# Optimization experiments

Measured on AMD Instinct MI355X. Metric: run time of the kernel, lower is better.

Reference implementation:

```python
import jax, jax.numpy as jnp
import numpy as np

# ---- config (matches init_kwargs) ----
B, L = 2, 4096
HID = 2048            # hidden_size
N_HEADS = 16          # (max_ngram_size-1) * n_head_per_ngram = 2*8
D_HEAD = 64           # n_embed_per_ngram // n_head_per_ngram
ENG = 1024            # (max_ngram_size-1) * n_embed_per_ngram
VOCAB = 129280        # per-head hash vocab
HC = 4                # hc_mult
K = 4                 # kernel_size
DIL = 3               # dilation = max_ngram_size
EPS_RMS = 1.1920929e-07   # torch RMSNorm default eps (fp32 finfo eps)
EPS_SC = 1e-05            # ShortConv RMSNorm eps


def setup_inputs() -> dict:
    key = jax.random.key(0)
    ks = jax.random.split(key, 10)
    hidden_states = jax.random.normal(ks[0], (B, L, HID), dtype=jnp.float32)
    hash_ids = jax.random.randint(ks[1], (B, L, N_HEADS), 0, VOCAB, dtype=jnp.int64)
    emb_tables = jax.random.normal(ks[2], (N_HEADS, VOCAB, D_HEAD), dtype=jnp.float32) * 0.02
    value_w = jax.random.normal(ks[3], (ENG, HID), dtype=jnp.float32) * (1.0 / np.sqrt(ENG))
    value_b = jnp.zeros((HID,), dtype=jnp.float32)
    key_w = jax.random.normal(ks[4], (HC, ENG, HID), dtype=jnp.float32) * (1.0 / np.sqrt(ENG))
    key_b = jnp.zeros((HC, HID), dtype=jnp.float32)
    norm1_w = jnp.ones((HC, HID), dtype=jnp.float32)
    norm2_w = jnp.ones((HC, HID), dtype=jnp.float32)
    sc_norm_w = jnp.ones((HC, HID), dtype=jnp.float32)
    conv_w = jax.random.normal(ks[5], (HC * HID, 1, K), dtype=jnp.float32) * (1.0 / np.sqrt(K))
    return {
        'hidden_states': hidden_states, 'hash_ids': hash_ids,
        'emb_tables': emb_tables, 'value_w': value_w, 'value_b': value_b,
        'key_w': key_w, 'key_b': key_b, 'norm1_w': norm1_w, 'norm2_w': norm2_w,
        'sc_norm_w': sc_norm_w, 'conv_w': conv_w,
    }


def _rms(x, w, eps):
    # x: [..., D], w broadcastable to x
    var = jnp.mean(x * x, axis=-1, keepdims=True)
    return x * jax.lax.rsqrt(var + eps) * w


def _short_conv(val, sc_norm_w, conv_w):
    # val: [B, L, HC, HID]
    xn = _rms(val, sc_norm_w[None, None, :, :], EPS_SC)          # per-channel RMSNorm
    x_bct = xn.reshape(B, L, HC * HID).transpose(0, 2, 1)        # [B, C, T]
    pad = (K - 1) * DIL                                          # causal left pad
    y = jax.lax.conv_general_dilated(
        x_bct, conv_w, window_strides=(1,), padding=[(pad, 0)],
        rhs_dilation=(DIL,), dimension_numbers=('NCH', 'OIH', 'NCH'),
        feature_group_count=HC * HID)                            # depthwise
    y = jax.nn.silu(y)
    return y.transpose(0, 2, 1).reshape(B, L, HC, HID)


def reference(hidden_states, hash_ids, emb_tables, value_w, value_b,
              key_w, key_b, norm1_w, norm2_w, sc_norm_w, conv_w):
    # multi-head embedding gather: per head its own table -> [B, L, H, Dh]
    emb = jax.vmap(lambda tab, ids: tab[ids], in_axes=(0, 2), out_axes=2)(emb_tables, hash_ids)
    emb = emb.reshape(B, L, ENG)                                 # flatten heads

    # per-channel key projections and gate computation
    keys = jnp.einsum('ble,geh->blgh', emb, key_w) + key_b[None, None]   # [B,L,HC,HID]
    nk = _rms(keys, norm1_w[None, None], EPS_RMS)
    nq = _rms(hidden_states[:, :, None, :], norm2_w[None, None], EPS_RMS)
    gate = jnp.sum(nk * nq, axis=-1) / np.sqrt(HID)              # [B,L,HC]
    gate = jnp.sign(gate) * jnp.sqrt(jnp.maximum(jnp.abs(gate), 1e-06))
    gate = jax.nn.sigmoid(gate)[..., None]                       # [B,L,HC,1]

    value = gate * (emb @ value_w + value_b)[:, :, None, :]      # [B,L,HC,HID]
    out = value + _short_conv(value, sc_norm_w, conv_w)
    return out.sum(axis=2)                                       # [B,L,HID]
```

## Files before the change

kernel.cpp:

```cpp
#include <hip/hip_runtime.h>
#include <math.h>

#define LQ 4096
#define MTOK 8192
#define HID 2048
#define NHEADS 16
#define DHEAD 64
#define ENG 1024
#define VOCAB 129280
#define HC 4
#define EPS_RMS 1.1920929e-07f
#define EPS_SC  1e-05f
#define INV_SQRT_HID 0.022097086912079608f

typedef __bf16 bf16;
typedef __attribute__((ext_vector_type(8))) __bf16 bf16x8;
typedef __attribute__((ext_vector_type(4))) __bf16 bf16x4;
typedef __attribute__((ext_vector_type(4))) float f32x4;

#define AS1 __attribute__((address_space(1)))
#define AS3 __attribute__((address_space(3)))

__device__ __forceinline__ void gl_lds16(const void* g, void* l) {
    __builtin_amdgcn_global_load_lds((const AS1 unsigned int*)g,
                                     (AS3 unsigned int*)l, 16, 0, 0);
}

__global__ __launch_bounds__(256) void gather_kernel(
        const int* __restrict__ hash_ids,
        const float* __restrict__ emb_tables,
        bf16* __restrict__ emb)
{
    int t = blockIdx.x;
    int tid = threadIdx.x;
    const int* ids = hash_ids + (size_t)t * NHEADS;
    int k = tid * 4;
    int h = k >> 6, d = k & 63;
    int id = ids[h];
    float4 v = *(const float4*)(emb_tables + ((size_t)h * VOCAB + (size_t)id) * DHEAD + d);
    bf16x4 o = {(bf16)v.x, (bf16)v.y, (bf16)v.z, (bf16)v.w};
    *(bf16x4*)(emb + (size_t)t * ENG + k) = o;
}

__global__ __launch_bounds__(256) void transpose_kernel(
        const float* __restrict__ value_w,
        const float* __restrict__ key_w,
        bf16* __restrict__ vwT,
        bf16* __restrict__ kwT)
{
    __shared__ float tile[32][33];
    int z = blockIdx.z;
    const float* src = (z == 0) ? value_w : key_w + (size_t)(z - 1) * ENG * HID;
    bf16* dst = (z == 0) ? vwT : kwT + (size_t)(z - 1) * HID * ENG;
    int c0 = blockIdx.x * 32, r0 = blockIdx.y * 32;
    int tx = threadIdx.x & 31, ty = threadIdx.x >> 5;
    #pragma unroll
    for (int i = 0; i < 4; ++i)
        tile[ty + i * 8][tx] = src[(size_t)(r0 + ty + i * 8) * HID + c0 + tx];
    __syncthreads();
    #pragma unroll
    for (int i = 0; i < 4; ++i)
        dst[(size_t)(c0 + ty + i * 8) * ENG + r0 + tx] = (bf16)tile[tx][ty + i * 8];
}

__global__ __launch_bounds__(256, 1) void gemm_value_mfma(
        const bf16* __restrict__ A,
        const bf16* __restrict__ Bt,
        const float* __restrict__ bias,
        float* __restrict__ C,
        float* __restrict__ pv2)
{
    __shared__ __align__(16) bf16 sA[128 * 64];
    __shared__ __align__(16) bf16 sB[128 * 64];
    int tid = threadIdx.x;
    int L = tid & 63, w = tid >> 6;
    int m0 = blockIdx.y * 128, n0 = blockIdx.x * 128;
    int mw = (w & 1) * 64, nw = (w >> 1) * 64;
    int lrow = L >> 3;
    int kcS = ((L & 7) ^ lrow) * 8;
    int lane15 = L & 15, quad = L >> 4;

    f32x4 acc[4][4];
    #pragma unroll
    for (int fm = 0; fm < 4; ++fm)
        #pragma unroll
        for (int fn = 0; fn < 4; ++fn)
            acc[fm][fn] = (f32x4){0.f, 0.f, 0.f, 0.f};

    for (int k0 = 0; k0 < ENG; k0 += 64) {
        #pragma unroll
        for (int i = 0; i < 4; ++i) {
            int seg = w * 4 + i;
            gl_lds16(A + (size_t)(m0 + seg * 8 + lrow) * ENG + k0 + kcS, sA + seg * 512);
            gl_lds16(Bt + (size_t)(n0 + seg * 8 + lrow) * ENG + k0 + kcS, sB + seg * 512);
        }
        __syncthreads();
        #pragma unroll
        for (int ks = 0; ks < 2; ++ks) {
            bf16x8 af[4], bfr[4];
            int kc = ks * 4 + quad;
            #pragma unroll
            for (int f = 0; f < 4; ++f) {
                int ra = mw + f * 16 + lane15;
                int rb = nw + f * 16 + lane15;
                af[f]  = *(const bf16x8*)(sA + ra * 64 + ((kc ^ (ra & 7)) * 8));
                bfr[f] = *(const bf16x8*)(sB + rb * 64 + ((kc ^ (rb & 7)) * 8));
            }
            #pragma unroll
            for (int fm = 0; fm < 4; ++fm)
                #pragma unroll
                for (int fn = 0; fn < 4; ++fn)
                    acc[fm][fn] = __builtin_amdgcn_mfma_f32_16x16x32_bf16(
                        af[fm], bfr[fn], acc[fm][fn], 0, 0, 0);
        }
        __syncthreads();
    }
    #pragma unroll
    for (int fm = 0; fm < 4; ++fm) {
        #pragma unroll
        for (int r = 0; r < 4; ++r) {
            int m = m0 + mw + fm * 16 + quad * 4 + r;
            float sv = 0.f;
            #pragma unroll
            for (int fn = 0; fn < 4; ++fn) {
                int n = n0 + nw + fn * 16 + lane15;
                float v = acc[fm][fn][r] + bias[n];
                C[(size_t)m * HID + n] = v;
                sv += v * v;
            }
            sv += __shfl_xor(sv, 1); sv += __shfl_xor(sv, 2);
            sv += __shfl_xor(sv, 4); sv += __shfl_xor(sv, 8);
            if (lane15 == 0) atomicAdd(&pv2[m], sv);
        }
    }
}

__global__ __launch_bounds__(256, 1) void gemm_keys_mfma(
        const bf16* __restrict__ A,
        const bf16* __restrict__ kwT,
        const float* __restrict__ key_b,
        const float* __restrict__ hidden,
        const float* __restrict__ w1,
        const float* __restrict__ w2,
        float* __restrict__ p_sq,
        float* __restrict__ p_dot)
{
    __shared__ __align__(16) bf16 sA[128 * 64];
    __shared__ __align__(16) bf16 sB[128 * 64];
    int tid = threadIdx.x;
    int L = tid & 63, w = tid >> 6;
    int m0 = blockIdx.y * 128;
    int c0 = blockIdx.x * 128;
    int g = c0 >> 11;
    int nc0 = c0 & (HID - 1);
    const bf16* Bt = kwT + (size_t)g * HID * ENG;
    int mw = (w & 1) * 64, nw = (w >> 1) * 64;
    int lrow = L >> 3;
    int kcS = ((L & 7) ^ lrow) * 8;
    int lane15 = L & 15, quad = L >> 4;

    f32x4 acc[4][4];
    #pragma unroll
    for (int fm = 0; fm < 4; ++fm)
        #pragma unroll
        for (int fn = 0; fn < 4; ++fn)
            acc[fm][fn] = (f32x4){0.f, 0.f, 0.f, 0.f};

    for (int k0 = 0; k0 < ENG; k0 += 64) {
        #pragma unroll
        for (int i = 0; i < 4; ++i) {
            int seg = w * 4 + i;
            gl_lds16(A  + (size_t)(m0  + seg * 8 + lrow) * ENG + k0 + kcS, sA + seg * 512);
            gl_lds16(Bt + (size_t)(nc0 + seg * 8 + lrow) * ENG + k0 + kcS, sB + seg * 512);
        }
        __syncthreads();
        #pragma unroll
        for (int ks = 0; ks < 2; ++ks) {
            bf16x8 af[4], bfr[4];
            int kc = ks * 4 + quad;
            #pragma unroll
            for (int f = 0; f < 4; ++f) {
                int ra = mw + f * 16 + lane15;
                int rb = nw + f * 16 + lane15;
                af[f]  = *(const bf16x8*)(sA + ra * 64 + ((kc ^ (ra & 7)) * 8));
                bfr[f] = *(const bf16x8*)(sB + rb * 64 + ((kc ^ (rb & 7)) * 8));
            }
            #pragma unroll
            for (int fm = 0; fm < 4; ++fm)
                #pragma unroll
                for (int fn = 0; fn < 4; ++fn)
                    acc[fm][fn] = __builtin_amdgcn_mfma_f32_16x16x32_bf16(
                        af[fm], bfr[fn], acc[fm][fn], 0, 0, 0);
        }
        __syncthreads();
    }
    const float* kb = key_b + (size_t)g * HID;
    const float* w1g = w1 + (size_t)g * HID;
    const float* w2g = w2 + (size_t)g * HID;
    #pragma unroll
    for (int fm = 0; fm < 4; ++fm) {
        #pragma unroll
        for (int r = 0; r < 4; ++r) {
            int m = m0 + mw + fm * 16 + quad * 4 + r;
            float psq = 0.f, pdt = 0.f;
            #pragma unroll
            for (int fn = 0; fn < 4; ++fn) {
                int nc = nc0 + nw + fn * 16 + lane15;
                float v = acc[fm][fn][r] + kb[nc];
                float hv = hidden[(size_t)m * HID + nc];
                float ww = w1g[nc] * w2g[nc];
                psq += v * v;
                pdt += v * hv * ww;
            }
            psq += __shfl_xor(psq, 1); psq += __shfl_xor(psq, 2);
            psq += __shfl_xor(psq, 4); psq += __shfl_xor(psq, 8);
            pdt += __shfl_xor(pdt, 1); pdt += __shfl_xor(pdt, 2);
            pdt += __shfl_xor(pdt, 4); pdt += __shfl_xor(pdt, 8);
            if (lane15 == 0) {
                atomicAdd(&p_sq[(size_t)m * HC + g], psq);
                atomicAdd(&p_dot[(size_t)m * HC + g], pdt);
            }
        }
    }
}

__global__ __launch_bounds__(256) void mq_kernel(
        const float* __restrict__ hidden, float* __restrict__ mq)
{
    int w = threadIdx.x >> 6, L = threadIdx.x & 63;
    int t = blockIdx.x * 4 + w;
    const float4* hp = (const float4*)(hidden + (size_t)t * HID);
    float s = 0.f;
    #pragma unroll
    for (int i = 0; i < 8; ++i) {
        float4 h = hp[L + i * 64];
        s += h.x * h.x + h.y * h.y + h.z * h.z + h.w * h.w;
    }
    #pragma unroll
    for (int msk = 1; msk < 64; msk <<= 1) s += __shfl_xor(s, msk);
    if (L == 0) mq[t] = s * (1.0f / HID);
}

__global__ __launch_bounds__(256) void finalize_kernel(
        const float* __restrict__ p_sq,
        const float* __restrict__ p_dot,
        const float* __restrict__ mq,
        const float* __restrict__ pv2,
        float* __restrict__ gate,
        float* __restrict__ cc)
{
    int i = blockIdx.x * 256 + threadIdx.x;
    if (i >= MTOK * HC) return;
    int t = i >> 2;
    float mk = p_sq[i] * (1.0f / HID) + EPS_RMS;
    float mqv = mq[t] + EPS_RMS;
    float raw = p_dot[i] * rsqrtf(mk) * rsqrtf(mqv) * INV_SQRT_HID;
    float g2 = copysignf(sqrtf(fmaxf(fabsf(raw), 1e-6f)), raw);
    float gt = 1.0f / (1.0f + expf(-g2));
    gate[i] = gt;
    float msqv = pv2[t] * (1.0f / HID);
    cc[i] = gt * rsqrtf(gt * gt * msqv + EPS_SC);
}

__global__ __launch_bounds__(256) void final_kernel(
        const float* __restrict__ vraw,
        const float* __restrict__ gate,
        const float* __restrict__ cc,
        const float* __restrict__ sc_w,
        const float* __restrict__ conv_w,
        float* __restrict__ out)
{
    int t = blockIdx.x;
    int l = t & (LQ - 1);
    int tid = threadIdx.x;
    float G = gate[t * 4 + 0] + gate[t * 4 + 1] + gate[t * 4 + 2] + gate[t * 4 + 3];
    float cg[4][4];
    int tki[4];
    #pragma unroll
    for (int k = 0; k < 4; ++k) {
        int lk = l + 3 * k - 9;
        bool valid = (lk >= 0);
        int tk = t + 3 * k - 9;
        tki[k] = valid ? tk : -1;
        #pragma unroll
        for (int g = 0; g < 4; ++g)
            cg[k][g] = valid ? cc[tk * 4 + g] : 0.0f;
    }
    #pragma unroll
    for (int i = 0; i < 2; ++i) {
        int h4 = tid + i * 256;
        float4 vk[4];
        #pragma unroll
        for (int k = 0; k < 4; ++k) {
            vk[k] = (tki[k] >= 0)
                  ? ((const float4*)(vraw + (size_t)tki[k] * HID))[h4]
                  : make_float4(0.f, 0.f, 0.f, 0.f);
        }
        float res[4];
        #pragma unroll
        for (int j = 0; j < 4; ++j) {
            int h = h4 * 4 + j;
            float vt = ((const float*)&vk[3])[j];
            float o = vt * G;
            #pragma unroll
            for (int g = 0; g < 4; ++g) {
                float4 w4 = ((const float4*)conv_w)[(size_t)g * HID + h];
                float y = w4.x * cg[0][g] * ((const float*)&vk[0])[j]
                        + w4.y * cg[1][g] * ((const float*)&vk[1])[j]
                        + w4.z * cg[2][g] * ((const float*)&vk[2])[j]
                        + w4.w * cg[3][g] * ((const float*)&vk[3])[j];
                y *= sc_w[(size_t)g * HID + h];
                o += y / (1.0f + expf(-y));
            }
            res[j] = o;
        }
        ((float4*)(out + (size_t)t * HID))[h4] = make_float4(res[0], res[1], res[2], res[3]);
    }
}

extern "C" void kernel_launch(void* const* d_in, const int* in_sizes, int n_in,
                              void* d_out, int out_size, void* d_ws, size_t ws_size,
                              hipStream_t stream)
{
    const float* hidden     = (const float*)d_in[0];
    const int*   hash_ids   = (const int*)  d_in[1];
    const float* emb_tables = (const float*)d_in[2];
    const float* value_w    = (const float*)d_in[3];
    const float* value_b    = (const float*)d_in[4];
    const float* key_w      = (const float*)d_in[5];
    const float* key_b      = (const float*)d_in[6];
    const float* norm1_w    = (const float*)d_in[7];
    const float* norm2_w    = (const float*)d_in[8];
    const float* sc_norm_w  = (const float*)d_in[9];
    const float* conv_w     = (const float*)d_in[10];
    float* out = (float*)d_out;

    char* ws = (char*)d_ws;
    bf16*  ws_emb  = (bf16*)ws;  ws += sizeof(bf16) * (size_t)MTOK * ENG;
    bf16*  ws_vwT  = (bf16*)ws;  ws += sizeof(bf16) * (size_t)HID * ENG;
    bf16*  ws_kwT  = (bf16*)ws;  ws += sizeof(bf16) * (size_t)HC * HID * ENG;
    float* ws_vraw = (float*)ws; ws += sizeof(float) * (size_t)MTOK * HID;
    float* ws_psq  = (float*)ws; ws += sizeof(float) * (size_t)MTOK * HC;
    float* ws_pdot = (float*)ws; ws += sizeof(float) * (size_t)MTOK * HC;
    float* ws_pv2  = (float*)ws; ws += sizeof(float) * (size_t)MTOK;
    float* ws_mq   = (float*)ws; ws += sizeof(float) * (size_t)MTOK;
    float* ws_gate = (float*)ws; ws += sizeof(float) * (size_t)MTOK * HC;
    float* ws_cc   = (float*)ws; ws += sizeof(float) * (size_t)MTOK * HC;

    hipMemsetAsync(ws_psq, 0, sizeof(float) * ((size_t)MTOK * HC * 2 + MTOK), stream);

    transpose_kernel<<<dim3(HID / 32, ENG / 32, 5), 256, 0, stream>>>(
        value_w, key_w, ws_vwT, ws_kwT);

    gather_kernel<<<MTOK, 256, 0, stream>>>(hash_ids, emb_tables, ws_emb);

    gemm_value_mfma<<<dim3(HID / 128, MTOK / 128), 256, 0, stream>>>(
        ws_emb, ws_vwT, value_b, ws_vraw, ws_pv2);

    gemm_keys_mfma<<<dim3(HC * HID / 128, MTOK / 128), 256, 0, stream>>>(
        ws_emb, ws_kwT, key_b, hidden, norm1_w, norm2_w, ws_psq, ws_pdot);

    mq_kernel<<<MTOK / 4, 256, 0, stream>>>(hidden, ws_mq);

    finalize_kernel<<<(MTOK * HC + 255) / 256, 256, 0, stream>>>(
        ws_psq, ws_pdot, ws_mq, ws_pv2, ws_gate, ws_cc);

    final_kernel<<<MTOK, 256, 0, stream>>>(
        ws_vraw, ws_gate, ws_cc, sc_norm_w, conv_w, out);
}
```

Measured before the change: 1.213 ms.

## Enlarge GEMM tiles to 256x256 with double-buffered LDS and swizzled block order

Both MFMA GEMMs move from 128x128 tiles with 4 waves to 256x256 tiles with 8 waves, each wave computing a 128x64 sub-tile. LDS is double-buffered so the next K-slice load overlaps the current MFMA compute, removing one barrier per iteration. Block IDs are remapped in groups of 8 for cache locality, and s_setprio raises priority around the MFMA bursts. This cuts global traffic per flop and hides load latency. In exchange it needs 128 KB of LDS and more accumulator registers per thread. With so few tiles the GPU may be under-filled, and the launch bounds of two blocks per CU may not hold.

```diff
diff --git a/kernel.cpp b/kernel.cpp
--- a/kernel.cpp
+++ b/kernel.cpp
@@ -63,67 +63,92 @@
         dst[(size_t)(c0 + ty + i * 8) * ENG + r0 + tx] = (bf16)tile[tx][ty + i * 8];
 }
 
-__global__ __launch_bounds__(256, 1) void gemm_value_mfma(
+__global__ __launch_bounds__(512, 2) void gemm_value_mfma(
         const bf16* __restrict__ A,
         const bf16* __restrict__ Bt,
         const float* __restrict__ bias,
         float* __restrict__ C,
         float* __restrict__ pv2)
 {
-    __shared__ __align__(16) bf16 sA[128 * 64];
-    __shared__ __align__(16) bf16 sB[128 * 64];
+    __shared__ __align__(16) bf16 sA[2][256 * 64];
+    __shared__ __align__(16) bf16 sB[2][256 * 64];
     int tid = threadIdx.x;
     int L = tid & 63, w = tid >> 6;
-    int m0 = blockIdx.y * 128, n0 = blockIdx.x * 128;
-    int mw = (w & 1) * 64, nw = (w >> 1) * 64;
+    int nwgx = gridDim.x;
+    int nwg  = nwgx * gridDim.y;
+    int bid  = blockIdx.y * nwgx + blockIdx.x;
+    int cpx  = nwg >> 3;
+    int swz  = (bid & 7) * cpx + (bid >> 3);
+    int m0 = (swz / nwgx) * 256;
+    int n0 = (swz % nwgx) * 256;
+    int wm = (w & 1) * 128, wn = (w >> 1) * 64;
     int lrow = L >> 3;
     int kcS = ((L & 7) ^ lrow) * 8;
     int lane15 = L & 15, quad = L >> 4;
 
-    f32x4 acc[4][4];
-    #pragma unroll
-    for (int fm = 0; fm < 4; ++fm)
+    f32x4 acc[8][4];
+    #pragma unroll
+    for (int fm = 0; fm < 8; ++fm)
         #pragma unroll
         for (int fn = 0; fn < 4; ++fn)
             acc[fm][fn] = (f32x4){0.f, 0.f, 0.f, 0.f};
 
-    for (int k0 = 0; k0 < ENG; k0 += 64) {
+    auto STAGE = [&](int buf, int k0) {
         #pragma unroll
         for (int i = 0; i < 4; ++i) {
             int seg = w * 4 + i;
-            gl_lds16(A + (size_t)(m0 + seg * 8 + lrow) * ENG + k0 + kcS, sA + seg * 512);
-            gl_lds16(Bt + (size_t)(n0 + seg * 8 + lrow) * ENG + k0 + kcS, sB + seg * 512);
-        }
-        __syncthreads();
+            gl_lds16(A  + (size_t)(m0 + seg * 8 + lrow) * ENG + k0 + kcS,
+                     &sA[buf][seg * 512]);
+            gl_lds16(Bt + (size_t)(n0 + seg * 8 + lrow) * ENG + k0 + kcS,
+                     &sB[buf][seg * 512]);
+        }
+    };
+    auto COMPUTE = [&](int buf) {
         #pragma unroll
         for (int ks = 0; ks < 2; ++ks) {
-            bf16x8 af[4], bfr[4];
+            bf16x8 af[8], bfr[4];
             int kc = ks * 4 + quad;
             #pragma unroll
+            for (int f = 0; f < 8; ++f) {
+                int ra = wm + f * 16 + lane15;
+                af[f] = *(const bf16x8*)(&sA[buf][ra * 64 + ((kc ^ (ra & 7)) * 8)]);
+            }
+            #pragma unroll
             for (int f = 0; f < 4; ++f) {
-                int ra = mw + f * 16 + lane15;
-                int rb = nw + f * 16 + lane15;
-                af[f]  = *(const bf16x8*)(sA + ra * 64 + ((kc ^ (ra & 7)) * 8));
-                bfr[f] = *(const bf16x8*)(sB + rb * 64 + ((kc ^ (rb & 7)) * 8));
-            }
-            #pragma unroll
-            for (int fm = 0; fm < 4; ++fm)
+                int rb = wn + f * 16 + lane15;
+                bfr[f] = *(const bf16x8*)(&sB[buf][rb * 64 + ((kc ^ (rb & 7)) * 8)]);
+            }
+            __builtin_amdgcn_s_setprio(1);
+            #pragma unroll
+            for (int fm = 0; fm < 8; ++fm)
                 #pragma unroll
                 for (int fn = 0; fn < 4; ++fn)
                     acc[fm][fn] = __builtin_amdgcn_mfma_f32_16x16x32_bf16(
                         af[fm], bfr[fn], acc[fm][fn], 0, 0, 0);
-        }
+            __builtin_amdgcn_s_setprio(0);
+        }
+    };
+
+    STAGE(0, 0);
+    __syncthreads();
+    int cur = 0;
+    for (int t = 0; t < ENG / 64 - 1; ++t) {
+        STAGE(cur ^ 1, (t + 1) * 64);
+        COMPUTE(cur);
         __syncthreads();
-    }
-    #pragma unroll
-    for (int fm = 0; fm < 4; ++fm) {
+        cur ^= 1;
+    }
+    COMPUTE(cur);
+
+    #pragma unroll
+    for (int fm = 0; fm < 8; ++fm) {
         #pragma unroll
         for (int r = 0; r < 4; ++r) {
-            int m = m0 + mw + fm * 16 + quad * 4 + r;
+            int m = m0 + wm + fm * 16 + quad * 4 + r;
             float sv = 0.f;
             #pragma unroll
             for (int fn = 0; fn < 4; ++fn) {
-                int n = n0 + nw + fn * 16 + lane15;
+                int n = n0 + wn + fn * 16 + lane15;
                 float v = acc[fm][fn][r] + bias[n];
                 C[(size_t)m * HID + n] = v;
                 sv += v * v;
@@ -135,7 +160,7 @@
     }
 }
 
-__global__ __launch_bounds__(256, 1) void gemm_keys_mfma(
+__global__ __launch_bounds__(512, 2) void gemm_keys_mfma(
         const bf16* __restrict__ A,
         const bf16* __restrict__ kwT,
         const float* __restrict__ key_b,
@@ -145,67 +170,91 @@
         float* __restrict__ p_sq,
         float* __restrict__ p_dot)
 {
-    __shared__ __align__(16) bf16 sA[128 * 64];
-    __shared__ __align__(16) bf16 sB[128 * 64];
+    __shared__ __align__(16) bf16 sA[2][256 * 64];
+    __shared__ __align__(16) bf16 sB[2][256 * 64];
     int tid = threadIdx.x;
     int L = tid & 63, w = tid >> 6;
-    int m0 = blockIdx.y * 128;
-    int c0 = blockIdx.x * 128;
-    int g = c0 >> 11;
+    int nwgx = gridDim.x;
+    int nwg  = nwgx * gridDim.y;
+    int bid  = blockIdx.y * nwgx + blockIdx.x;
+    int cpx  = nwg >> 3;
+    int swz  = (bid & 7) * cpx + (bid >> 3);
+    int m0 = (swz / nwgx) * 256;
+    int c0 = (swz % nwgx) * 256;
+    int g   = c0 >> 11;
     int nc0 = c0 & (HID - 1);
     const bf16* Bt = kwT + (size_t)g * HID * ENG;
-    int mw = (w & 1) * 64, nw = (w >> 1) * 64;
+    int wm = (w & 1) * 128, wn = (w >> 1) * 64;
     int lrow = L >> 3;
     int kcS = ((L & 7) ^ lrow) * 8;
     int lane15 = L & 15, quad = L >> 4;
 
-    f32x4 acc[4][4];
-    #pragma unroll
-    for (int fm = 0; fm < 4; ++fm)
+    f32x4 acc[8][4];
+    #pragma unroll
+    for (int fm = 0; fm < 8; ++fm)
         #pragma unroll
         for (int fn = 0; fn < 4; ++fn)
             acc[fm][fn] = (f32x4){0.f, 0.f, 0.f, 0.f};
 
-    for (int k0 = 0; k0 < ENG; k0 += 64) {
+    auto STAGE = [&](int buf, int k0) {
         #pragma unroll
         for (int i = 0; i < 4; ++i) {
             int seg = w * 4 + i;
-            gl_lds16(A  + (size_t)(m0  + seg * 8 + lrow) * ENG + k0 + kcS, sA + seg * 512);
-            gl_lds16(Bt + (size_t)(nc0 + seg * 8 + lrow) * ENG + k0 + kcS, sB + seg * 512);
-        }
-        __syncthreads();
+            gl_lds16(A  + (size_t)(m0  + seg * 8 + lrow) * ENG + k0 + kcS,
+                     &sA[buf][seg * 512]);
+            gl_lds16(Bt + (size_t)(nc0 + seg * 8 + lrow) * ENG + k0 + kcS,
+                     &sB[buf][seg * 512]);
+        }
+    };
+    auto COMPUTE = [&](int buf) {
         #pragma unroll
         for (int ks = 0; ks < 2; ++ks) {
-            bf16x8 af[4], bfr[4];
+            bf16x8 af[8], bfr[4];
             int kc = ks * 4 + quad;
             #pragma unroll
+            for (int f = 0; f < 8; ++f) {
+                int ra = wm + f * 16 + lane15;
+                af[f] = *(const bf16x8*)(&sA[buf][ra * 64 + ((kc ^ (ra & 7)) * 8)]);
+            }
+            #pragma unroll
             for (int f = 0; f < 4; ++f) {
-                int ra = mw + f * 16 + lane15;
-                int rb = nw + f * 16 + lane15;
-                af[f]  = *(const bf16x8*)(sA + ra * 64 + ((kc ^ (ra & 7)) * 8));
-                bfr[f] = *(const bf16x8*)(sB + rb * 64 + ((kc ^ (rb & 7)) * 8));
-            }
-            #pragma unroll
-            for (int fm = 0; fm < 4; ++fm)
+                int rb = wn + f * 16 + lane15;
+                bfr[f] = *(const bf16x8*)(&sB[buf][rb * 64 + ((kc ^ (rb & 7)) * 8)]);
+            }
+            __builtin_amdgcn_s_setprio(1);
+            #pragma unroll
+            for (int fm = 0; fm < 8; ++fm)
                 #pragma unroll
                 for (int fn = 0; fn < 4; ++fn)
                     acc[fm][fn] = __builtin_amdgcn_mfma_f32_16x16x32_bf16(
                         af[fm], bfr[fn], acc[fm][fn], 0, 0, 0);
-        }
+            __builtin_amdgcn_s_setprio(0);
+        }
+    };
+
+    STAGE(0, 0);
+    __syncthreads();
+    int cur = 0;
+    for (int t = 0; t < ENG / 64 - 1; ++t) {
+        STAGE(cur ^ 1, (t + 1) * 64);
+        COMPUTE(cur);
         __syncthreads();
-    }
-    const float* kb = key_b + (size_t)g * HID;
+        cur ^= 1;
+    }
+    COMPUTE(cur);
+
+    const float* kb  = key_b + (size_t)g * HID;
     const float* w1g = w1 + (size_t)g * HID;
     const float* w2g = w2 + (size_t)g * HID;
     #pragma unroll
-    for (int fm = 0; fm < 4; ++fm) {
+    for (int fm = 0; fm < 8; ++fm) {
         #pragma unroll
         for (int r = 0; r < 4; ++r) {
-            int m = m0 + mw + fm * 16 + quad * 4 + r;
+            int m = m0 + wm + fm * 16 + quad * 4 + r;
             float psq = 0.f, pdt = 0.f;
             #pragma unroll
             for (int fn = 0; fn < 4; ++fn) {
-                int nc = nc0 + nw + fn * 16 + lane15;
+                int nc = nc0 + wn + fn * 16 + lane15;
                 float v = acc[fm][fn][r] + kb[nc];
                 float hv = hidden[(size_t)m * HID + nc];
                 float ww = w1g[nc] * w2g[nc];
@@ -354,10 +403,10 @@
 
     gather_kernel<<<MTOK, 256, 0, stream>>>(hash_ids, emb_tables, ws_emb);
 
-    gemm_value_mfma<<<dim3(HID / 128, MTOK / 128), 256, 0, stream>>>(
+    gemm_value_mfma<<<dim3(HID / 256, MTOK / 256), 512, 0, stream>>>(
         ws_emb, ws_vwT, value_b, ws_vraw, ws_pv2);
 
-    gemm_keys_mfma<<<dim3(HC * HID / 128, MTOK / 128), 256, 0, stream>>>(
+    gemm_keys_mfma<<<dim3(HC * HID / 256, MTOK / 256), 512, 0, stream>>>(
         ws_emb, ws_kwT, key_b, hidden, norm1_w, norm2_w, ws_psq, ws_pdot);
 
     mq_kernel<<<MTOK / 4, 256, 0, stream>>>(hidden, ws_mq);
```

New measurement: 1.401 ms. 15.5% more time.
